# Kernel tuning notes

Measured on AMD Instinct MI355X. Metric: run time of the kernel, lower is better.

The kernel has to match this reference:

```python
import jax, jax.numpy as jnp
import numpy as np

N_NODES = 100000
N_EDGES = 800000
# (in_dim, out_channels_per_head, heads) for the 5 stacked GATConv layers
DIMS = [(32, 24, 10), (240, 24, 5), (120, 24, 2), (48, 24, 1), (24, 12, 1)]
NEG_SLOPE = 0.2  # PyG GATConv default leaky_relu slope


def setup_inputs() -> dict:
    key = jax.random.key(0)
    ks = jax.random.split(key, 4 + 4 * len(DIMS))
    x = jax.random.normal(ks[0], (N_NODES, 32), jnp.float32)
    # edge_index with no self loops (dst = src + nonzero offset mod N),
    # since PyG GATConv removes then re-adds self loops.
    src = jax.random.randint(ks[1], (N_EDGES,), 0, N_NODES)
    off = jax.random.randint(ks[2], (N_EDGES,), 1, N_NODES)
    dst = (src + off) % N_NODES
    edge_index = jnp.stack([src, dst]).astype(jnp.int32)
    edge_attr = jax.random.normal(ks[3], (N_EDGES, 4), jnp.float32)
    inp = {"x": x, "edge_index": edge_index, "edge_attr": edge_attr}
    for i, (din, c, h) in enumerate(DIMS):
        kw, kb, ka, kd = ks[4 + 4 * i: 8 + 4 * i]
        s = 1.0 / np.sqrt(din)
        inp[f"W{i}"] = jax.random.normal(kw, (din, h * c), jnp.float32) * s
        inp[f"b{i}"] = jax.random.normal(kb, (h * c,), jnp.float32) * 0.01
        inp[f"as{i}"] = jax.random.normal(ka, (h, c), jnp.float32) * (1.0 / np.sqrt(c))
        inp[f"ad{i}"] = jax.random.normal(kd, (h, c), jnp.float32) * (1.0 / np.sqrt(c))
    return inp


def gat_layer(x, src, dst, W, b, a_src, a_dst):
    # Faithful PyG GATConv (concat=True, bias=True, edge_dim=None)
    n = x.shape[0]
    h_heads, c = a_src.shape
    h = (x @ W).reshape(n, h_heads, c)                      # [N,H,C]
    alpha_s = jnp.einsum('nhc,hc->nh', h, a_src)            # [N,H]
    alpha_d = jnp.einsum('nhc,hc->nh', h, a_dst)            # [N,H]
    e = jax.nn.leaky_relu(alpha_s[src] + alpha_d[dst], NEG_SLOPE)  # [E,H]
    # segment softmax over incoming edges of each destination node
    m = jax.ops.segment_max(e, dst, num_segments=n)         # [N,H]
    ex = jnp.exp(e - m[dst])
    z = jax.ops.segment_sum(ex, dst, num_segments=n)        # [N,H]
    attn = ex / z[dst]                                      # [E,H]
    out = jax.ops.segment_sum(h[src] * attn[:, :, None], dst, num_segments=n)
    return out.reshape(n, h_heads * c) + b


def reference(x, edge_index, edge_attr,
              W0, b0, as0, ad0, W1, b1, as1, ad1, W2, b2, as2, ad2,
              W3, b3, as3, ad3, W4, b4, as4, ad4):
    # edge_attr is ignored: GATConv(edge_dim=None) does not use it.
    n = x.shape[0]
    loop = jnp.arange(n, dtype=edge_index.dtype)
    src = jnp.concatenate([edge_index[0], loop])  # add self loops (PyG default)
    dst = jnp.concatenate([edge_index[1], loop])
    params = [(W0, b0, as0, ad0), (W1, b1, as1, ad1), (W2, b2, as2, ad2),
              (W3, b3, as3, ad3), (W4, b4, as4, ad4)]
    for W, b, a_s, a_d in params:
        x = jax.nn.relu(gat_layer(x, src, dst, W, b, a_s, a_d))
    return x
```

## Files before the change

kernel.cpp:

```cpp
#include <hip/hip_runtime.h>
#include <math.h>

#define NN 100000
#define EE 800000
#define ET (EE + NN)
#define BS 256
#define BKTS 391
#define FB_EPB 4096
#define LDSCAP 4096

typedef _Float16 f16;
typedef __attribute__((ext_vector_type(4))) _Float16 half4;
typedef __attribute__((ext_vector_type(8))) _Float16 half8;
typedef __attribute__((ext_vector_type(4))) float f32x4;
template<int V> struct HV;
template<> struct HV<4>{ typedef half4 type; };
template<> struct HV<8>{ typedef half8 type; };

static inline int cdiv(long a, int b){ return (int)((a + b - 1) / b); }

__global__ __launch_bounds__(256) void k_bhist(const int* __restrict__ ei,
                                               int* __restrict__ bucketCount){
    __shared__ int hist[BKTS];
    for (int t = threadIdx.x; t < BKTS; t += 256) hist[t] = 0;
    __syncthreads();
    const int e0 = blockIdx.x * FB_EPB + threadIdx.x;
    #pragma unroll
    for (int i = 0; i < 16; i++){
        int e = e0 + i * 256;
        if (e < ET){
            int d = (e < EE) ? ei[EE + e] : (e - EE);
            atomicAdd(&hist[d >> 8], 1);
        }
    }
    __syncthreads();
    for (int t = threadIdx.x; t < BKTS; t += 256){
        int c = hist[t];
        if (c) atomicAdd(&bucketCount[t], c);
    }
}

__global__ void k_bscan(const int* __restrict__ bucketCount, int* __restrict__ bucketBase,
                        int* __restrict__ bucketCursor, int* __restrict__ rowptr){
    __shared__ int sh[512];
    int t = threadIdx.x;
    int c = (t < BKTS) ? bucketCount[t] : 0;
    sh[t] = c;
    __syncthreads();
    for (int o = 1; o < 512; o <<= 1){
        int v = (t >= o) ? sh[t - o] : 0;
        __syncthreads();
        sh[t] += v;
        __syncthreads();
    }
    if (t < BKTS){
        int excl = sh[t] - c;
        bucketBase[t] = excl;
        bucketCursor[t] = excl;
    }
    if (t == 0){
        bucketBase[BKTS] = ET;
        rowptr[NN] = ET;
    }
}

__global__ __launch_bounds__(256) void k_bfill(const int* __restrict__ ei,
        int* __restrict__ bucketCursor, unsigned* __restrict__ bpack){
    __shared__ int hist[BKTS];
    __shared__ int base[BKTS];
    for (int t = threadIdx.x; t < BKTS; t += 256) hist[t] = 0;
    __syncthreads();
    const int e0 = blockIdx.x * FB_EPB + threadIdx.x;
    unsigned pk[16], rb[16];
    #pragma unroll
    for (int i = 0; i < 16; i++){
        int e = e0 + i * 256;
        rb[i] = 0xFFFFFFFFu;
        if (e < ET){
            int s, d;
            if (e < EE){ s = ei[e]; d = ei[EE + e]; } else { s = e - EE; d = s; }
            int b = d >> 8;
            int r = atomicAdd(&hist[b], 1);
            pk[i] = ((unsigned)(d & 255) << 17) | (unsigned)s;
            rb[i] = ((unsigned)r << 9) | (unsigned)b;
        }
    }
    __syncthreads();
    for (int t = threadIdx.x; t < BKTS; t += 256){
        int c = hist[t];
        base[t] = c ? atomicAdd(&bucketCursor[t], c) : 0;
    }
    __syncthreads();
    #pragma unroll
    for (int i = 0; i < 16; i++){
        if (rb[i] != 0xFFFFFFFFu){
            int b = rb[i] & 511;
            int r = rb[i] >> 9;
            bpack[base[b] + r] = pk[i];
        }
    }
}

__global__ __launch_bounds__(256) void k_bsort(const unsigned* __restrict__ bpack,
        const int* __restrict__ bucketBase, int* __restrict__ rowptr,
        int* __restrict__ ssrc, int* __restrict__ sdst){
    __shared__ int cnt[256];
    __shared__ int off[256];
    __shared__ unsigned stage[LDSCAP];
    int b = blockIdx.x;
    int n0 = bucketBase[b], n1 = bucketBase[b + 1];
    int nE = n1 - n0;
    int t = threadIdx.x;
    cnt[t] = 0;
    __syncthreads();
    for (int i = t; i < nE; i += 256){
        unsigned v = bpack[n0 + i];
        atomicAdd(&cnt[v >> 17], 1);
    }
    __syncthreads();
    int cv = cnt[t];
    off[t] = cv;
    __syncthreads();
    for (int o = 1; o < 256; o <<= 1){
        int v = (t >= o) ? off[t - o] : 0;
        __syncthreads();
        off[t] += v;
        __syncthreads();
    }
    int excl = off[t] - cv;
    __syncthreads();
    off[t] = excl;
    cnt[t] = 0;
    __syncthreads();
    for (int i = t; i < nE; i += 256){
        unsigned v = bpack[n0 + i];
        int dl = v >> 17;
        int r = atomicAdd(&cnt[dl], 1);
        stage[off[dl] + r] = v;
    }
    int d = b * 256 + t;
    if (d < NN) rowptr[d] = n0 + excl;
    __syncthreads();
    for (int i = t; i < nE; i += 256){
        unsigned v = stage[i];
        ssrc[n0 + i] = (int)(v & 0x1FFFFu);
        sdst[n0 + i] = b * 256 + (int)(v >> 17);
    }
}

template<int K, int M, int KP, int MP, int HH, int CC>
__device__ __forceinline__ void prep_one(int idx, const float* __restrict__ W,
        const float* __restrict__ b, const float* __restrict__ as_,
        const float* __restrict__ ad_, f16* __restrict__ Wpk,
        float* __restrict__ bp, float* __restrict__ Was, float* __restrict__ Wad){
    constexpr int NT = MP / 16;
    if (idx < KP * MP){
        int j    = idx & 7;
        int lane = (idx >> 3) & 63;
        int rest = idx >> 9;
        int nt   = rest % NT;
        int ks   = rest / NT;
        int k = ks * 32 + ((lane >> 4) & 3) * 8 + j;
        int n = nt * 16 + (lane & 15);
        Wpk[idx] = (k < K && n < M) ? (f16)W[k * M + n] : (f16)0.f;
    }
    if (idx < MP) bp[idx] = (idx < M) ? b[idx] : 0.f;
    if (idx < K * HH){
        int k = idx / HH, hd = idx - k * HH;
        float s = 0.f, d = 0.f;
        #pragma unroll
        for (int c = 0; c < CC; c++){
            float w = W[k * M + hd * CC + c];
            s = fmaf(w, as_[hd * CC + c], s);
            d = fmaf(w, ad_[hd * CC + c], d);
        }
        Was[idx] = s;
        Wad[idx] = d;
    }
}

__device__ __forceinline__ void prep_w0(int idx, const float* __restrict__ W0,
                                        f16* __restrict__ Wpk0){
    int j    = idx & 7;
    int lane = (idx >> 3) & 63;
    int nt   = (idx >> 9) & 1;
    int hd   = idx >> 10;
    int k    = ((lane >> 4) & 3) * 8 + j;
    int cih  = nt * 16 + (lane & 15);
    Wpk0[idx] = (cih < 24) ? (f16)W0[k * 240 + hd * 24 + cih] : (f16)0.f;
}

struct PrepAll {
    const float *W[5], *b[5], *as[5], *ad[5];
    f16*   Wpk[5];
    f16*   Wpk0;
    float* bp[5];
    float* Was[5];
    float* Wad[5];
    int*   bucketCount;
};

__global__ void k_prep_all(PrepAll a){
    int idx = blockIdx.x * 256 + threadIdx.x;
    if (idx < 7680)
        prep_one< 32, 240,  32, 240, 10, 24>(idx,         a.W[0], a.b[0], a.as[0], a.ad[0], a.Wpk[0], a.bp[0], a.Was[0], a.Wad[0]);
    else if (idx < 40448)
        prep_one<240, 120, 256, 128,  5, 24>(idx - 7680,  a.W[1], a.b[1], a.as[1], a.ad[1], a.Wpk[1], a.bp[1], a.Was[1], a.Wad[1]);
    else if (idx < 48640)
        prep_one<120,  48, 128,  64,  2, 24>(idx - 40448, a.W[2], a.b[2], a.as[2], a.ad[2], a.Wpk[2], a.bp[2], a.Was[2], a.Wad[2]);
    else if (idx < 50688)
        prep_one< 48,  24,  64,  32,  1, 24>(idx - 48640, a.W[3], a.b[3], a.as[3], a.ad[3], a.Wpk[3], a.bp[3], a.Was[3], a.Wad[3]);
    else if (idx < 51200)
        prep_one< 24,  12,  32,  16,  1, 12>(idx - 50688, a.W[4], a.b[4], a.as[4], a.ad[4], a.Wpk[4], a.bp[4], a.Was[4], a.Wad[4]);
    else if (idx < 61440)
        prep_w0(idx - 51200, a.W[0], a.Wpk0);
    else if (idx < 61440 + BKTS)
        a.bucketCount[idx - 61440] = 0;
}

__global__ void k_cvt_alpha0(const float* __restrict__ X, f16* __restrict__ Xh,
                             const float* __restrict__ Was, const float* __restrict__ Wad,
                             float* __restrict__ als, float* __restrict__ ald){
    int n = blockIdx.x * BS + threadIdx.x;
    if (n >= NN) return;
    float xr[32];
    #pragma unroll
    for (int i = 0; i < 8; i++){
        float4 v = *(const float4*)(X + (long)n * 32 + i * 4);
        xr[i * 4 + 0] = v.x; xr[i * 4 + 1] = v.y;
        xr[i * 4 + 2] = v.z; xr[i * 4 + 3] = v.w;
    }
    #pragma unroll
    for (int i = 0; i < 4; i++){
        half8 h;
        #pragma unroll
        for (int c = 0; c < 8; c++) h[c] = (f16)xr[i * 8 + c];
        *(half8*)(Xh + (long)n * 32 + i * 8) = h;
    }
    float s[10] = {}, d[10] = {};
    for (int k = 0; k < 32; k++){
        float x = xr[k];
        #pragma unroll
        for (int hd = 0; hd < 10; hd++){
            s[hd] = fmaf(x, Was[k * 10 + hd], s[hd]);
            d[hd] = fmaf(x, Wad[k * 10 + hd], d[hd]);
        }
    }
    #pragma unroll
    for (int hd = 0; hd < 10; hd++){
        als[n * 10 + hd] = s[hd];
        ald[n * 10 + hd] = d[hd];
    }
}

template<int MPH, int HH, int CC>
__global__ void k_alpha_h(const f16* __restrict__ H2, const float* __restrict__ as_,
                          const float* __restrict__ ad_, float* __restrict__ als,
                          float* __restrict__ ald){
    int n = blockIdx.x * BS + threadIdx.x;
    if (n >= NN) return;
    const f16* h = H2 + (long)n * MPH;
    #pragma unroll
    for (int hd = 0; hd < HH; hd++){
        float s = 0.f, d = 0.f;
        #pragma unroll
        for (int c0 = 0; c0 < CC; c0 += 4){
            half4 hv = *(const half4*)(h + hd * CC + c0);
            #pragma unroll
            for (int j = 0; j < 4; j++){
                float hvf = (float)hv[j];
                s = fmaf(hvf, as_[hd * CC + c0 + j], s);
                d = fmaf(hvf, ad_[hd * CC + c0 + j], d);
            }
        }
        als[n * HH + hd] = s;
        ald[n * HH + hd] = d;
    }
}

template<int HH>
__global__ void k_mz2(const float* __restrict__ als, const float* __restrict__ ald,
                      const int* __restrict__ rowptr, const int* __restrict__ ssrc,
                      float* __restrict__ marr, float* __restrict__ zinvarr){
    int idx = blockIdx.x * BS + threadIdx.x;
    if (idx >= NN * HH) return;
    int n = idx / HH, hd = idx - n * HH;
    float adv = ald[idx];
    int beg = rowptr[n], end = rowptr[n + 1];
    float ma = -1e30f;
    for (int p = beg; p < end; p++)
        ma = fmaxf(ma, als[ssrc[p] * HH + hd]);
    float m = ma + adv;
    m = (m >= 0.f) ? m : 0.2f * m;
    float z = 0.f;
    for (int p = beg; p < end; p++){
        float e = als[ssrc[p] * HH + hd] + adv;
        e = (e >= 0.f) ? e : 0.2f * e;
        z += __expf(e - m);
    }
    marr[idx] = m;
    zinvarr[idx] = 1.f / z;
}

template<int HH, int ATTS, bool GROUPED>
__global__ __launch_bounds__(256) void k_att_edge(const float* __restrict__ als,
        const float* __restrict__ ald, const float* __restrict__ marr,
        const float* __restrict__ zinv, const int* __restrict__ ssrc,
        const int* __restrict__ sdst, f16* __restrict__ att){
    int p = blockIdx.x * 256 + threadIdx.x;
    if (p >= ET) return;
    int s = ssrc[p], d = sdst[p];
    float w[HH];
    #pragma unroll
    for (int hd = 0; hd < HH; hd++){
        float e = als[s * HH + hd] + ald[d * HH + hd];
        e = (e >= 0.f) ? e : 0.2f * e;
        w[hd] = __expf(e - marr[d * HH + hd]) * zinv[d * HH + hd];
    }
    if constexpr (GROUPED){
        half8 lo = {}, hi = {};
        #pragma unroll
        for (int h = 0; h < 5; h++){ lo[h] = (f16)w[h]; hi[h] = (f16)w[h + 5]; }
        *(half8*)(att + (long)p * 16)     = lo;
        *(half8*)(att + (long)p * 16 + 8) = hi;
    } else {
        half8 v = {};
        #pragma unroll
        for (int h = 0; h < HH; h++) v[h] = (f16)w[h];
        *(half8*)(att + (long)p * ATTS) = v;
    }
}

template<int HH, int ATTS>
__global__ void k_mz_att(const float* __restrict__ als, const float* __restrict__ ald,
                         const int* __restrict__ rowptr, const int* __restrict__ ssrc,
                         f16* __restrict__ att){
    int idx = blockIdx.x * BS + threadIdx.x;
    if (idx >= NN * HH) return;
    int n = idx / HH, hd = idx - n * HH;
    float adv = ald[idx];
    int beg = rowptr[n], end = rowptr[n + 1];
    float ma = -1e30f;
    for (int p = beg; p < end; p++)
        ma = fmaxf(ma, als[ssrc[p] * HH + hd]);
    float m = ma + adv;
    m = (m >= 0.f) ? m : 0.2f * m;
    float z = 0.f;
    for (int p = beg; p < end; p++){
        float e = als[ssrc[p] * HH + hd] + adv;
        e = (e >= 0.f) ? e : 0.2f * e;
        z += __expf(e - m);
    }
    float zinv = 1.f / z;
    for (int p = beg; p < end; p++){
        float e = als[ssrc[p] * HH + hd] + adv;
        e = (e >= 0.f) ? e : 0.2f * e;
        att[(long)p * ATTS + hd] = (f16)(__expf(e - m) * zinv);
    }
}

__global__ __launch_bounds__(256) void k_aggX0_gemm(const f16* __restrict__ Xh,
        const f16* __restrict__ att, const int* __restrict__ rowptr,
        const int* __restrict__ ssrc, const f16* __restrict__ Wpk0,
        const float* __restrict__ bp0, f16* __restrict__ X1){
    constexpr int SA = 328;
    constexpr int SO = 264;
    __shared__ f16 smem[32 * SA];
    const int t = threadIdx.x;
    const long n0 = (long)blockIdx.x * 32;

    {
        const int nloc = t >> 3;
        const int hg   = (t >> 2) & 1;
        const int ch   = t & 3;
        const int n    = (int)n0 + nloc;
        float acc[5][8] = {};
        int beg = rowptr[n], end = rowptr[n + 1];
        int p = beg;
        for (; p + 2 <= end; p += 2){
            int s0 = ssrc[p], s1 = ssrc[p + 1];
            half8 x0 = *(const half8*)(Xh + (long)s0 * 32 + ch * 8);
            half8 x1 = *(const half8*)(Xh + (long)s1 * 32 + ch * 8);
            half8 a0 = *(const half8*)(att + (long)p * 16 + hg * 8);
            half8 a1 = *(const half8*)(att + (long)(p + 1) * 16 + hg * 8);
            #pragma unroll
            for (int h = 0; h < 5; h++){
                float w0 = (float)a0[h], w1 = (float)a1[h];
                #pragma unroll
                for (int c = 0; c < 8; c++){
                    acc[h][c] = fmaf(w0, (float)x0[c], acc[h][c]);
                    acc[h][c] = fmaf(w1, (float)x1[c], acc[h][c]);
                }
            }
        }
        if (p < end){
            int s = ssrc[p];
            half8 xv = *(const half8*)(Xh + (long)s * 32 + ch * 8);
            half8 av = *(const half8*)(att + (long)p * 16 + hg * 8);
            #pragma unroll
            for (int h = 0; h < 5; h++){
                float w = (float)av[h];
                #pragma unroll
                for (int c = 0; c < 8; c++)
                    acc[h][c] = fmaf(w, (float)xv[c], acc[h][c]);
            }
        }
        #pragma unroll
        for (int h = 0; h < 5; h++){
            half8 o;
            #pragma unroll
            for (int c = 0; c < 8; c++) o[c] = (f16)acc[h][c];
            *(half8*)(smem + nloc * SA + (hg * 5 + h) * 32 + ch * 8) = o;
        }
    }
    __syncthreads();

    const int wave = t >> 6;
    const int lane = t & 63;
    const int quad = lane >> 4;
    const int l16  = lane & 15;
    const int mt   = wave & 1;
    half8 afr[5];
    #pragma unroll
    for (int i = 0; i < 5; i++){
        const int hd = (wave + 4 * i) >> 1;
        afr[i] = *(const half8*)(smem + (mt * 16 + l16) * SA + hd * 32 + quad * 8);
    }
    __syncthreads();
    #pragma unroll
    for (int i = 0; i < 5; i++){
        const int hd = (wave + 4 * i) >> 1;
        #pragma unroll
        for (int nt = 0; nt < 2; nt++){
            half8 bfr = *(const half8*)(Wpk0 + ((hd * 2 + nt) * 64 + lane) * 8);
            f32x4 acc2 = (f32x4){0.f, 0.f, 0.f, 0.f};
            acc2 = __builtin_amdgcn_mfma_f32_16x16x32_f16(afr[i], bfr, acc2, 0, 0, 0);
            int cih = nt * 16 + l16;
            if (cih < 24){
                float bv = bp0[hd * 24 + cih];
                #pragma unroll
                for (int reg = 0; reg < 4; reg++){
                    int rl = mt * 16 + quad * 4 + reg;
                    float v = acc2[reg] + bv;
                    smem[rl * SO + hd * 24 + cih] = (f16)((v > 0.f) ? v : 0.f);
                }
            }
        }
    }
    __syncthreads();

    const half8 hz = {};
    #pragma unroll
    for (int c = t; c < 1024; c += 256){
        int row = c >> 5, c8 = c & 31;
        half8 v = (c8 >= 30) ? hz : *(const half8*)(smem + row * SO + c8 * 8);
        *(half8*)(X1 + (n0 + row) * 256 + c8 * 8) = v;
    }
}

template<int KP, int MPH>
__global__ __launch_bounds__(256) void k_gemm_mfma(const f16* __restrict__ Xh,
        const f16* __restrict__ Wpk, f16* __restrict__ H2){
    constexpr int NT = MPH / 16;
    constexpr int KS = KP / 32;
    const int wave = threadIdx.x >> 6;
    const int lane = threadIdx.x & 63;
    const int quad = lane >> 4;
    const int l16  = lane & 15;
    const long row0 = (long)blockIdx.x * 128 + wave * 32;

    f32x4 acc[2][NT];
    #pragma unroll
    for (int mt = 0; mt < 2; mt++)
        #pragma unroll
        for (int nt = 0; nt < NT; nt++)
            acc[mt][nt] = (f32x4){0.f, 0.f, 0.f, 0.f};

    const long r0 = row0 + l16;
    const long r1 = row0 + 16 + l16;
    const half8 hz = {};
    half8 a0 = (r0 < NN) ? *(const half8*)(Xh + r0 * KP + quad * 8) : hz;
    half8 a1 = (r1 < NN) ? *(const half8*)(Xh + r1 * KP + quad * 8) : hz;
    half8 bc[NT];
    #pragma unroll
    for (int nt = 0; nt < NT; nt++)
        bc[nt] = *(const half8*)(Wpk + ((long)nt * 64 + lane) * 8);

    for (int ks = 0; ks < KS; ks++){
        half8 n0 = hz, n1 = hz, bn[NT];
        if (ks + 1 < KS){
            const int kk = (ks + 1) * 32 + quad * 8;
            n0 = (r0 < NN) ? *(const half8*)(Xh + r0 * KP + kk) : hz;
            n1 = (r1 < NN) ? *(const half8*)(Xh + r1 * KP + kk) : hz;
            const f16* bp_ = Wpk + ((long)(ks + 1) * NT * 64 + lane) * 8;
            #pragma unroll
            for (int nt = 0; nt < NT; nt++)
                bn[nt] = *(const half8*)(bp_ + (long)nt * 512);
        } else {
            #pragma unroll
            for (int nt = 0; nt < NT; nt++) bn[nt] = hz;
        }
        #pragma unroll
        for (int nt = 0; nt < NT; nt++){
            acc[0][nt] = __builtin_amdgcn_mfma_f32_16x16x32_f16(a0, bc[nt], acc[0][nt], 0, 0, 0);
            acc[1][nt] = __builtin_amdgcn_mfma_f32_16x16x32_f16(a1, bc[nt], acc[1][nt], 0, 0, 0);
        }
        a0 = n0; a1 = n1;
        #pragma unroll
        for (int nt = 0; nt < NT; nt++) bc[nt] = bn[nt];
    }
    #pragma unroll
    for (int mt = 0; mt < 2; mt++){
        #pragma unroll
        for (int reg = 0; reg < 4; reg++){
            long r = row0 + mt * 16 + quad * 4 + reg;
            if (r < NN){
                #pragma unroll
                for (int nt = 0; nt < NT; nt++)
                    H2[r * MPH + nt * 16 + l16] = (f16)acc[mt][nt][reg];
            }
        }
    }
}

template<int HH, int CC, int ATTS, int MPH, int MPO, int VEC, bool O16>
__global__ __launch_bounds__(256) void k_agg_h(const f16* __restrict__ H2,
        const f16* __restrict__ att,
        const int* __restrict__ rowptr, const int* __restrict__ ssrc,
        const float* __restrict__ bp, f16* __restrict__ out16,
        float* __restrict__ out32, int MREAL){
    constexpr int TPN = MPO / VEC;
    typedef typename HV<VEC>::type hvec;
    int idx = blockIdx.x * 256 + threadIdx.x;
    if (idx >= NN * TPN) return;
    int n = idx / TPN;
    int q = idx - n * TPN;
    int j0 = q * VEC;
    if constexpr (O16 && (MPO > MPH)){
        if (j0 >= MPH){
            hvec zv = {};
            *(hvec*)(out16 + (long)n * MPO + j0) = zv;
            return;
        }
    }
    int hd = j0 / CC; if (hd > HH - 1) hd = HH - 1;

    int beg = rowptr[n], end = rowptr[n + 1];
    float acc[VEC] = {};
    int p = beg;
    for (; p + 2 <= end; p += 2){
        int s0 = ssrc[p], s1 = ssrc[p + 1];
        float w0 = (float)att[(long)p * ATTS + hd];
        float w1 = (float)att[(long)(p + 1) * ATTS + hd];
        hvec h0 = *(const hvec*)(H2 + (long)s0 * MPH + j0);
        hvec h1 = *(const hvec*)(H2 + (long)s1 * MPH + j0);
        #pragma unroll
        for (int c = 0; c < VEC; c++){
            acc[c] = fmaf(w0, (float)h0[c], acc[c]);
            acc[c] = fmaf(w1, (float)h1[c], acc[c]);
        }
    }
    if (p < end){
        int s = ssrc[p];
        float w = (float)att[(long)p * ATTS + hd];
        hvec hv = *(const hvec*)(H2 + (long)s * MPH + j0);
        #pragma unroll
        for (int c = 0; c < VEC; c++)
            acc[c] = fmaf(w, (float)hv[c], acc[c]);
    }
    if constexpr (O16){
        hvec o;
        #pragma unroll
        for (int c = 0; c < VEC; c++){
            float v = acc[c] + bp[j0 + c];
            o[c] = (f16)((v > 0.f) ? v : 0.f);
        }
        *(hvec*)(out16 + (long)n * MPO + j0) = o;
    } else {
        if (j0 < MREAL){
            #pragma unroll
            for (int c = 0; c < VEC; c++){
                float v = acc[c] + bp[j0 + c];
                out32[(long)n * MREAL + j0 + c] = (v > 0.f) ? v : 0.f;
            }
        }
    }
}

template<int K, int M, int KP, int MPH, int MPO, int HH, int CC, int ATTS, int VEC,
         bool O16, bool EDGEATT>
static void run_layer(const f16* Xh, f16* H2, f16* att,
                      const f16* Wpk, const float* bp,
                      const float* asv, const float* adv,
                      float* als, float* ald, float* marr, float* zinv,
                      const int* rowptr, const int* ssrc, const int* sdst,
                      f16* Xnext, float* out32, hipStream_t stream){
    constexpr int TPN = MPO / VEC;
    k_gemm_mfma<KP, MPH><<<cdiv(NN, 128), 256, 0, stream>>>(Xh, Wpk, H2);
    k_alpha_h<MPH, HH, CC><<<cdiv(NN, BS), BS, 0, stream>>>(H2, asv, adv, als, ald);
    if constexpr (EDGEATT){
        k_mz2<HH><<<cdiv((long)NN * HH, BS), BS, 0, stream>>>(als, ald, rowptr, ssrc, marr, zinv);
        k_att_edge<HH, ATTS, false><<<cdiv(ET, 256), 256, 0, stream>>>(
            als, ald, marr, zinv, ssrc, sdst, att);
    } else {
        k_mz_att<HH, ATTS><<<cdiv((long)NN * HH, BS), BS, 0, stream>>>(
            als, ald, rowptr, ssrc, att);
    }
    k_agg_h<HH, CC, ATTS, MPH, MPO, VEC, O16><<<cdiv((long)NN * TPN, 256), 256, 0, stream>>>(
        H2, att, rowptr, ssrc, bp, Xnext, out32, M);
}

extern "C" void kernel_launch(void* const* d_in, const int* in_sizes, int n_in,
                              void* d_out, int out_size, void* d_ws, size_t ws_size,
                              hipStream_t stream){
    const float* x0 = (const float*)d_in[0];
    const int*   ei = (const int*)d_in[1];
    PrepAll pa;
    for (int i = 0; i < 5; i++){
        pa.W[i]  = (const float*)d_in[3 + 4 * i];
        pa.b[i]  = (const float*)d_in[4 + 4 * i];
        pa.as[i] = (const float*)d_in[5 + 4 * i];
        pa.ad[i] = (const float*)d_in[6 + 4 * i];
    }

    char* p = (char*)d_ws;
    auto alloc = [&](size_t bytes) -> char* {
        char* r = p;
        p += (bytes + 255) & ~(size_t)255;
        return r;
    };
    f16*   Xh     = (f16*)alloc((size_t)NN * 256 * 2);
    f16*   H2     = (f16*)alloc((size_t)NN * 320 * 2);
    f16*   att    = (f16*)alloc((size_t)ET * 16 * 2);
    float* als    = (float*)alloc((size_t)NN * 10 * 4);
    float* ald    = (float*)alloc((size_t)NN * 10 * 4);
    float* marr   = (float*)alloc((size_t)NN * 10 * 4);
    float* zinv   = (float*)alloc((size_t)NN * 10 * 4);
    const int wpkSz[5] = {7680, 32768, 8192, 2048, 512};
    const int mpSz[5]  = {240, 128, 64, 32, 16};
    const int khSz[5]  = {320, 1200, 240, 48, 24};
    for (int i = 0; i < 5; i++){
        pa.Wpk[i] = (f16*)alloc((size_t)wpkSz[i] * 2);
        pa.bp[i]  = (float*)alloc((size_t)mpSz[i] * 4);
        pa.Was[i] = (float*)alloc((size_t)khSz[i] * 4);
        pa.Wad[i] = (float*)alloc((size_t)khSz[i] * 4);
    }
    pa.Wpk0 = (f16*)alloc((size_t)10240 * 2);
    int*      bucketCount  = (int*)alloc((size_t)BKTS * 4);
    int*      bucketBase   = (int*)alloc((size_t)(BKTS + 1) * 4);
    int*      bucketCursor = (int*)alloc((size_t)BKTS * 4);
    unsigned* bpack        = (unsigned*)alloc((size_t)ET * 4);
    int*      rowptr       = (int*)alloc((size_t)(NN + 1) * 4);
    int*      ssrc         = (int*)alloc((size_t)ET * 4);
    int*      sdst         = (int*)alloc((size_t)ET * 4);
    pa.bucketCount = bucketCount;

    k_prep_all<<<242, 256, 0, stream>>>(pa);
    k_bhist<<<cdiv(ET, FB_EPB), 256, 0, stream>>>(ei, bucketCount);
    k_bscan<<<1, 512, 0, stream>>>(bucketCount, bucketBase, bucketCursor, rowptr);
    k_bfill<<<cdiv(ET, FB_EPB), 256, 0, stream>>>(ei, bucketCursor, bpack);
    k_bsort<<<BKTS, 256, 0, stream>>>(bpack, bucketBase, rowptr, ssrc, sdst);

    k_cvt_alpha0<<<cdiv(NN, BS), BS, 0, stream>>>(x0, Xh, pa.Was[0], pa.Wad[0], als, ald);
    k_mz2<10><<<cdiv((long)NN * 10, BS), BS, 0, stream>>>(als, ald, rowptr, ssrc, marr, zinv);
    k_att_edge<10, 16, true><<<cdiv(ET, 256), 256, 0, stream>>>(
        als, ald, marr, zinv, ssrc, sdst, att);
    k_aggX0_gemm<<<NN / 32, 256, 0, stream>>>(Xh, att, rowptr, ssrc,
        pa.Wpk0, pa.bp[0], H2 );

    run_layer<240, 120, 256, 128, 128,  5, 24, 8, 8, true,  true >(H2, Xh, att, pa.Wpk[1],
        pa.bp[1], pa.as[1], pa.ad[1], als, ald, marr, zinv, rowptr, ssrc, sdst, H2, nullptr, stream);
    run_layer<120,  48, 128,  64,  64,  2, 24, 2, 8, true,  false>(H2, Xh, att, pa.Wpk[2],
        pa.bp[2], pa.as[2], pa.ad[2], als, ald, marr, zinv, rowptr, ssrc, sdst, H2, nullptr, stream);
    run_layer< 48,  24,  64,  32,  32,  1, 24, 1, 8, true,  false>(H2, Xh, att, pa.Wpk[3],
        pa.bp[3], pa.as[3], pa.ad[3], als, ald, marr, zinv, rowptr, ssrc, sdst, H2, nullptr, stream);
    run_layer< 24,  12,  32,  16,  16,  1, 12, 1, 4, false, false>(H2, Xh, att, pa.Wpk[4],
        pa.bp[4], pa.as[4], pa.ad[4], als, ald, marr, zinv, rowptr, ssrc, sdst, nullptr, (float*)d_out, stream);
}
```

Before: 505.0 us.

## Fuse segment softmax into one per-node online-softmax kernel and drop sdst

Replaces the separate max/sum kernel plus per-edge attention kernel (and the per-head k_mz_att) with a single per-node kernel. One thread per destination node computes all heads with an online max/sum recurrence, then writes normalized attention weights. This removes the marr/zinv and sdst arrays and two launches. als/ald rows are padded to 12 floats so they can be read with vector loads. The layer-0 aggregation loop is also unrolled by four. The trade-off is fewer threads (one per node, 64-thread blocks) with serial per-node edge loops and extra exp work in the online update.

```diff
diff --git a/kernel.cpp b/kernel.cpp
--- a/kernel.cpp
+++ b/kernel.cpp
@@ -10,6 +10,7 @@
 #define LDSCAP 4096
 
 typedef _Float16 f16;
+typedef __attribute__((ext_vector_type(2))) _Float16 h2v;
 typedef __attribute__((ext_vector_type(4))) _Float16 half4;
 typedef __attribute__((ext_vector_type(8))) _Float16 half8;
 typedef __attribute__((ext_vector_type(4))) float f32x4;
@@ -103,7 +104,7 @@
 
 __global__ __launch_bounds__(256) void k_bsort(const unsigned* __restrict__ bpack,
         const int* __restrict__ bucketBase, int* __restrict__ rowptr,
-        int* __restrict__ ssrc, int* __restrict__ sdst){
+        int* __restrict__ ssrc){
     __shared__ int cnt[256];
     __shared__ int off[256];
     __shared__ unsigned stage[LDSCAP];
@@ -144,7 +145,6 @@
     for (int i = t; i < nE; i += 256){
         unsigned v = stage[i];
         ssrc[n0 + i] = (int)(v & 0x1FFFFu);
-        sdst[n0 + i] = b * 256 + (int)(v >> 17);
     }
 }
 
@@ -248,12 +248,12 @@
     }
     #pragma unroll
     for (int hd = 0; hd < 10; hd++){
-        als[n * 10 + hd] = s[hd];
-        ald[n * 10 + hd] = d[hd];
-    }
-}
-
-template<int MPH, int HH, int CC>
+        als[(long)n * 12 + hd] = s[hd];
+        ald[(long)n * 12 + hd] = d[hd];
+    }
+}
+
+template<int MPH, int HH, int CC, int SL>
 __global__ void k_alpha_h(const f16* __restrict__ H2, const float* __restrict__ as_,
                           const float* __restrict__ ad_, float* __restrict__ als,
                           float* __restrict__ ald){
@@ -273,89 +273,108 @@
                 d = fmaf(hvf, ad_[hd * CC + c0 + j], d);
             }
         }
-        als[n * HH + hd] = s;
-        ald[n * HH + hd] = d;
-    }
-}
-
-template<int HH>
-__global__ void k_mz2(const float* __restrict__ als, const float* __restrict__ ald,
-                      const int* __restrict__ rowptr, const int* __restrict__ ssrc,
-                      float* __restrict__ marr, float* __restrict__ zinvarr){
-    int idx = blockIdx.x * BS + threadIdx.x;
-    if (idx >= NN * HH) return;
-    int n = idx / HH, hd = idx - n * HH;
-    float adv = ald[idx];
-    int beg = rowptr[n], end = rowptr[n + 1];
-    float ma = -1e30f;
-    for (int p = beg; p < end; p++)
-        ma = fmaxf(ma, als[ssrc[p] * HH + hd]);
-    float m = ma + adv;
-    m = (m >= 0.f) ? m : 0.2f * m;
-    float z = 0.f;
-    for (int p = beg; p < end; p++){
-        float e = als[ssrc[p] * HH + hd] + adv;
-        e = (e >= 0.f) ? e : 0.2f * e;
-        z += __expf(e - m);
-    }
-    marr[idx] = m;
-    zinvarr[idx] = 1.f / z;
-}
-
-template<int HH, int ATTS, bool GROUPED>
-__global__ __launch_bounds__(256) void k_att_edge(const float* __restrict__ als,
-        const float* __restrict__ ald, const float* __restrict__ marr,
-        const float* __restrict__ zinv, const int* __restrict__ ssrc,
-        const int* __restrict__ sdst, f16* __restrict__ att){
-    int p = blockIdx.x * 256 + threadIdx.x;
-    if (p >= ET) return;
-    int s = ssrc[p], d = sdst[p];
-    float w[HH];
-    #pragma unroll
-    for (int hd = 0; hd < HH; hd++){
-        float e = als[s * HH + hd] + ald[d * HH + hd];
-        e = (e >= 0.f) ? e : 0.2f * e;
-        w[hd] = __expf(e - marr[d * HH + hd]) * zinv[d * HH + hd];
-    }
-    if constexpr (GROUPED){
-        half8 lo = {}, hi = {};
-        #pragma unroll
-        for (int h = 0; h < 5; h++){ lo[h] = (f16)w[h]; hi[h] = (f16)w[h + 5]; }
-        *(half8*)(att + (long)p * 16)     = lo;
-        *(half8*)(att + (long)p * 16 + 8) = hi;
+        als[(long)n * SL + hd] = s;
+        ald[(long)n * SL + hd] = d;
+    }
+}
+
+template<int HH, int SL>
+__device__ __forceinline__ void load_row(const float* __restrict__ base, long s,
+                                         float* __restrict__ e){
+    const float* r = base + s * SL;
+    if constexpr (HH == 10){
+        float4 a = *(const float4*)r;
+        float4 b = *(const float4*)(r + 4);
+        float2 c = *(const float2*)(r + 8);
+        e[0]=a.x; e[1]=a.y; e[2]=a.z; e[3]=a.w;
+        e[4]=b.x; e[5]=b.y; e[6]=b.z; e[7]=b.w;
+        e[8]=c.x; e[9]=c.y;
+    } else if constexpr (HH == 5){
+        float4 a = *(const float4*)r;
+        e[0]=a.x; e[1]=a.y; e[2]=a.z; e[3]=a.w; e[4]=r[4];
+    } else if constexpr (HH == 2){
+        float2 a = *(const float2*)r;
+        e[0]=a.x; e[1]=a.y;
     } else {
-        half8 v = {};
-        #pragma unroll
-        for (int h = 0; h < HH; h++) v[h] = (f16)w[h];
-        *(half8*)(att + (long)p * ATTS) = v;
-    }
-}
-
-template<int HH, int ATTS>
-__global__ void k_mz_att(const float* __restrict__ als, const float* __restrict__ ald,
-                         const int* __restrict__ rowptr, const int* __restrict__ ssrc,
-                         f16* __restrict__ att){
-    int idx = blockIdx.x * BS + threadIdx.x;
-    if (idx >= NN * HH) return;
-    int n = idx / HH, hd = idx - n * HH;
-    float adv = ald[idx];
-    int beg = rowptr[n], end = rowptr[n + 1];
-    float ma = -1e30f;
-    for (int p = beg; p < end; p++)
-        ma = fmaxf(ma, als[ssrc[p] * HH + hd]);
-    float m = ma + adv;
-    m = (m >= 0.f) ? m : 0.2f * m;
-    float z = 0.f;
-    for (int p = beg; p < end; p++){
-        float e = als[ssrc[p] * HH + hd] + adv;
-        e = (e >= 0.f) ? e : 0.2f * e;
-        z += __expf(e - m);
-    }
-    float zinv = 1.f / z;
-    for (int p = beg; p < end; p++){
-        float e = als[ssrc[p] * HH + hd] + adv;
-        e = (e >= 0.f) ? e : 0.2f * e;
-        att[(long)p * ATTS + hd] = (f16)(__expf(e - m) * zinv);
+        e[0]=r[0];
+    }
+}
+
+__device__ __forceinline__ void smx_upd(float& ma, float& L, float& z, float e, float adv){
+    float mn = fmaxf(ma, e);
+    float Ln = mn + adv; Ln = (Ln >= 0.f) ? Ln : 0.2f * Ln;
+    float ev = e + adv;  ev = (ev >= 0.f) ? ev : 0.2f * ev;
+    z = z * __expf(L - Ln) + __expf(ev - Ln);
+    ma = mn; L = Ln;
+}
+
+template<int HH, int SL, int ATTS>
+__global__ __launch_bounds__(64) void k_mzatt_node(const float* __restrict__ als,
+        const float* __restrict__ ald, const int* __restrict__ rowptr,
+        const int* __restrict__ ssrc, f16* __restrict__ att){
+    int n = blockIdx.x * 64 + threadIdx.x;
+    if (n >= NN) return;
+    float adv[HH], ma[HH], L[HH], z[HH];
+    {
+        float tmp[HH];
+        load_row<HH, SL>(ald, n, tmp);
+        #pragma unroll
+        for (int h = 0; h < HH; h++){
+            adv[h] = tmp[h]; ma[h] = -1e30f; L[h] = -1e30f; z[h] = 0.f;
+        }
+    }
+    const int beg = rowptr[n], end = rowptr[n + 1];
+    int p = beg;
+    for (; p + 4 <= end; p += 4){
+        int s0 = ssrc[p], s1 = ssrc[p+1], s2 = ssrc[p+2], s3 = ssrc[p+3];
+        float e0[HH], e1[HH], e2[HH], e3[HH];
+        load_row<HH, SL>(als, s0, e0);
+        load_row<HH, SL>(als, s1, e1);
+        load_row<HH, SL>(als, s2, e2);
+        load_row<HH, SL>(als, s3, e3);
+        #pragma unroll
+        for (int h = 0; h < HH; h++){
+            smx_upd(ma[h], L[h], z[h], e0[h], adv[h]);
+            smx_upd(ma[h], L[h], z[h], e1[h], adv[h]);
+            smx_upd(ma[h], L[h], z[h], e2[h], adv[h]);
+            smx_upd(ma[h], L[h], z[h], e3[h], adv[h]);
+        }
+    }
+    for (; p < end; ++p){
+        float e[HH];
+        load_row<HH, SL>(als, (long)ssrc[p], e);
+        #pragma unroll
+        for (int h = 0; h < HH; h++) smx_upd(ma[h], L[h], z[h], e[h], adv[h]);
+    }
+    float zi[HH];
+    #pragma unroll
+    for (int h = 0; h < HH; h++) zi[h] = 1.f / z[h];
+    for (p = beg; p < end; ++p){
+        float e[HH];
+        load_row<HH, SL>(als, (long)ssrc[p], e);
+        float w[HH];
+        #pragma unroll
+        for (int h = 0; h < HH; h++){
+            float ev = e[h] + adv[h]; ev = (ev >= 0.f) ? ev : 0.2f * ev;
+            w[h] = __expf(ev - L[h]) * zi[h];
+        }
+        if constexpr (HH == 10){
+            half8 lo = {}, hi = {};
+            #pragma unroll
+            for (int h = 0; h < 5; h++){ lo[h] = (f16)w[h]; hi[h] = (f16)w[h + 5]; }
+            *(half8*)(att + (long)p * 16)     = lo;
+            *(half8*)(att + (long)p * 16 + 8) = hi;
+        } else if constexpr (HH == 5){
+            half8 v = {};
+            #pragma unroll
+            for (int h = 0; h < 5; h++) v[h] = (f16)w[h];
+            *(half8*)(att + (long)p * 8) = v;
+        } else if constexpr (HH == 2){
+            h2v v; v[0] = (f16)w[0]; v[1] = (f16)w[1];
+            *(h2v*)(att + (long)p * 2) = v;
+        } else {
+            att[p] = (f16)w[0];
+        }
     }
 }
 
@@ -377,23 +396,30 @@
         float acc[5][8] = {};
         int beg = rowptr[n], end = rowptr[n + 1];
         int p = beg;
-        for (; p + 2 <= end; p += 2){
-            int s0 = ssrc[p], s1 = ssrc[p + 1];
+        for (; p + 4 <= end; p += 4){
+            int s0 = ssrc[p], s1 = ssrc[p+1], s2 = ssrc[p+2], s3 = ssrc[p+3];
             half8 x0 = *(const half8*)(Xh + (long)s0 * 32 + ch * 8);
             half8 x1 = *(const half8*)(Xh + (long)s1 * 32 + ch * 8);
+            half8 x2 = *(const half8*)(Xh + (long)s2 * 32 + ch * 8);
+            half8 x3 = *(const half8*)(Xh + (long)s3 * 32 + ch * 8);
             half8 a0 = *(const half8*)(att + (long)p * 16 + hg * 8);
-            half8 a1 = *(const half8*)(att + (long)(p + 1) * 16 + hg * 8);
+            half8 a1 = *(const half8*)(att + (long)(p+1) * 16 + hg * 8);
+            half8 a2 = *(const half8*)(att + (long)(p+2) * 16 + hg * 8);
+            half8 a3 = *(const half8*)(att + (long)(p+3) * 16 + hg * 8);
             #pragma unroll
             for (int h = 0; h < 5; h++){
                 float w0 = (float)a0[h], w1 = (float)a1[h];
+                float w2 = (float)a2[h], w3 = (float)a3[h];
                 #pragma unroll
                 for (int c = 0; c < 8; c++){
                     acc[h][c] = fmaf(w0, (float)x0[c], acc[h][c]);
                     acc[h][c] = fmaf(w1, (float)x1[c], acc[h][c]);
+                    acc[h][c] = fmaf(w2, (float)x2[c], acc[h][c]);
+                    acc[h][c] = fmaf(w3, (float)x3[c], acc[h][c]);
                 }
             }
         }
-        if (p < end){
+        for (; p < end; ++p){
             int s = ssrc[p];
             half8 xv = *(const half8*)(Xh + (long)s * 32 + ch * 8);
             half8 av = *(const half8*)(att + (long)p * 16 + hg * 8);
@@ -588,24 +614,17 @@
 }
 
 template<int K, int M, int KP, int MPH, int MPO, int HH, int CC, int ATTS, int VEC,
-         bool O16, bool EDGEATT>
-static void run_layer(const f16* Xh, f16* H2, f16* att,
+         bool O16, int SL>
+static void run_layer(const f16* Xin, f16* H2, f16* att,
                       const f16* Wpk, const float* bp,
                       const float* asv, const float* adv,
-                      float* als, float* ald, float* marr, float* zinv,
-                      const int* rowptr, const int* ssrc, const int* sdst,
+                      float* als, float* ald,
+                      const int* rowptr, const int* ssrc,
                       f16* Xnext, float* out32, hipStream_t stream){
     constexpr int TPN = MPO / VEC;
-    k_gemm_mfma<KP, MPH><<<cdiv(NN, 128), 256, 0, stream>>>(Xh, Wpk, H2);
-    k_alpha_h<MPH, HH, CC><<<cdiv(NN, BS), BS, 0, stream>>>(H2, asv, adv, als, ald);
-    if constexpr (EDGEATT){
-        k_mz2<HH><<<cdiv((long)NN * HH, BS), BS, 0, stream>>>(als, ald, rowptr, ssrc, marr, zinv);
-        k_att_edge<HH, ATTS, false><<<cdiv(ET, 256), 256, 0, stream>>>(
-            als, ald, marr, zinv, ssrc, sdst, att);
-    } else {
-        k_mz_att<HH, ATTS><<<cdiv((long)NN * HH, BS), BS, 0, stream>>>(
-            als, ald, rowptr, ssrc, att);
-    }
+    k_gemm_mfma<KP, MPH><<<cdiv(NN, 128), 256, 0, stream>>>(Xin, Wpk, H2);
+    k_alpha_h<MPH, HH, CC, SL><<<cdiv(NN, BS), BS, 0, stream>>>(H2, asv, adv, als, ald);
+    k_mzatt_node<HH, SL, ATTS><<<cdiv(NN, 64), 64, 0, stream>>>(als, ald, rowptr, ssrc, att);
     k_agg_h<HH, CC, ATTS, MPH, MPO, VEC, O16><<<cdiv((long)NN * TPN, 256), 256, 0, stream>>>(
         H2, att, rowptr, ssrc, bp, Xnext, out32, M);
 }
@@ -632,10 +651,8 @@
     f16*   Xh     = (f16*)alloc((size_t)NN * 256 * 2);
     f16*   H2     = (f16*)alloc((size_t)NN * 320 * 2);
     f16*   att    = (f16*)alloc((size_t)ET * 16 * 2);
-    float* als    = (float*)alloc((size_t)NN * 10 * 4);
-    float* ald    = (float*)alloc((size_t)NN * 10 * 4);
-    float* marr   = (float*)alloc((size_t)NN * 10 * 4);
-    float* zinv   = (float*)alloc((size_t)NN * 10 * 4);
+    float* als    = (float*)alloc((size_t)NN * 12 * 4);
+    float* ald    = (float*)alloc((size_t)NN * 12 * 4);
     const int wpkSz[5] = {7680, 32768, 8192, 2048, 512};
     const int mpSz[5]  = {240, 128, 64, 32, 16};
     const int khSz[5]  = {320, 1200, 240, 48, 24};
@@ -652,28 +669,25 @@
     unsigned* bpack        = (unsigned*)alloc((size_t)ET * 4);
     int*      rowptr       = (int*)alloc((size_t)(NN + 1) * 4);
     int*      ssrc         = (int*)alloc((size_t)ET * 4);
-    int*      sdst         = (int*)alloc((size_t)ET * 4);
     pa.bucketCount = bucketCount;
 
     k_prep_all<<<242, 256, 0, stream>>>(pa);
     k_bhist<<<cdiv(ET, FB_EPB), 256, 0, stream>>>(ei, bucketCount);
     k_bscan<<<1, 512, 0, stream>>>(bucketCount, bucketBase, bucketCursor, rowptr);
     k_bfill<<<cdiv(ET, FB_EPB), 256, 0, stream>>>(ei, bucketCursor, bpack);
-    k_bsort<<<BKTS, 256, 0, stream>>>(bpack, bucketBase, rowptr, ssrc, sdst);
+    k_bsort<<<BKTS, 256, 0, stream>>>(bpack, bucketBase, rowptr, ssrc);
 
     k_cvt_alpha0<<<cdiv(NN, BS), BS, 0, stream>>>(x0, Xh, pa.Was[0], pa.Wad[0], als, ald);
-    k_mz2<10><<<cdiv((long)NN * 10, BS), BS, 0, stream>>>(als, ald, rowptr, ssrc, marr, zinv);
-    k_att_edge<10, 16, true><<<cdiv(ET, 256), 256, 0, stream>>>(
-        als, ald, marr, zinv, ssrc, sdst, att);
+    k_mzatt_node<10, 12, 16><<<cdiv(NN, 64), 64, 0, stream>>>(als, ald, rowptr, ssrc, att);
     k_aggX0_gemm<<<NN / 32, 256, 0, stream>>>(Xh, att, rowptr, ssrc,
         pa.Wpk0, pa.bp[0], H2 );
 
-    run_layer<240, 120, 256, 128, 128,  5, 24, 8, 8, true,  true >(H2, Xh, att, pa.Wpk[1],
-        pa.bp[1], pa.as[1], pa.ad[1], als, ald, marr, zinv, rowptr, ssrc, sdst, H2, nullptr, stream);
-    run_layer<120,  48, 128,  64,  64,  2, 24, 2, 8, true,  false>(H2, Xh, att, pa.Wpk[2],
-        pa.bp[2], pa.as[2], pa.ad[2], als, ald, marr, zinv, rowptr, ssrc, sdst, H2, nullptr, stream);
-    run_layer< 48,  24,  64,  32,  32,  1, 24, 1, 8, true,  false>(H2, Xh, att, pa.Wpk[3],
-        pa.bp[3], pa.as[3], pa.ad[3], als, ald, marr, zinv, rowptr, ssrc, sdst, H2, nullptr, stream);
-    run_layer< 24,  12,  32,  16,  16,  1, 12, 1, 4, false, false>(H2, Xh, att, pa.Wpk[4],
-        pa.bp[4], pa.as[4], pa.ad[4], als, ald, marr, zinv, rowptr, ssrc, sdst, nullptr, (float*)d_out, stream);
-}
+    run_layer<240, 120, 256, 128, 128,  5, 24, 8, 8, true,  8>(H2, Xh, att, pa.Wpk[1],
+        pa.bp[1], pa.as[1], pa.ad[1], als, ald, rowptr, ssrc, H2, nullptr, stream);
+    run_layer<120,  48, 128,  64,  64,  2, 24, 2, 8, true,  2>(H2, Xh, att, pa.Wpk[2],
+        pa.bp[2], pa.as[2], pa.ad[2], als, ald, rowptr, ssrc, H2, nullptr, stream);
+    run_layer< 48,  24,  64,  32,  32,  1, 24, 1, 8, true,  1>(H2, Xh, att, pa.Wpk[3],
+        pa.bp[3], pa.as[3], pa.ad[3], als, ald, rowptr, ssrc, H2, nullptr, stream);
+    run_layer< 24,  12,  32,  16,  16,  1, 12, 1, 4, false, 1>(H2, Xh, att, pa.Wpk[4],
+        pa.bp[4], pa.as[4], pa.ad[4], als, ald, rowptr, ssrc, nullptr, (float*)d_out, stream);
+}
```

Measured after the change: 485.9 us. -3.8%, faster.
